# Kernel optimization log

Hardware: AMD Instinct MI355X
Metric: run time of the kernel (lower is better)

The kernel has to match this reference:

```python
import jax, jax.numpy as jnp
import numpy as np

B, N, C = 2, 10000, 128
NH, NP = 4, 20          # n_heads, n_points (n_levels = 1)
DH = C // NH            # head dim = 32
HW = 100                # spatial shape (100, 100), N = HW*HW


def setup_inputs() -> dict:
    key = jax.random.key(0)
    ks = jax.random.split(key, 12)
    s = 0.05  # small param scale so softmax/linears stay well-conditioned
    return {
        "query": jax.random.normal(ks[0], (B, N, C), jnp.float32),
        "query_pos": jax.random.normal(ks[1], (B, N, C), jnp.float32),
        "W_val": jax.random.normal(ks[2], (C, C), jnp.float32) * s,
        "b_val": jax.random.normal(ks[3], (C,), jnp.float32) * s,
        "W_off": jax.random.normal(ks[4], (NH * NP * 2, C), jnp.float32) * s,
        "b_off": jax.random.normal(ks[5], (NH * NP * 2,), jnp.float32) * s,
        "W_attn": jax.random.normal(ks[6], (NH * NP, C), jnp.float32) * s,
        "b_attn": jax.random.normal(ks[7], (NH * NP,), jnp.float32) * s,
        "W_out1": jax.random.normal(ks[8], (C, C), jnp.float32) * s,
        "b_out1": jax.random.normal(ks[9], (C,), jnp.float32) * s,
        "W_out2": jax.random.normal(ks[10], (C, C), jnp.float32) * s,
        "b_out2": jax.random.normal(ks[11], (C,), jnp.float32) * s,
    }


def _msdeform_forward(query, query_pos, W_val, b_val, W_off, b_off,
                      W_attn, b_attn, W_out1, b_out1, W_out2, b_out2):
    residual = query
    q = query + query_pos  # pos added; value branch also uses q (query.clone())

    # reference points: meshgrid of (z, x) normalized to (0,1), shape (N, 2)
    lin = (jnp.arange(HW, dtype=jnp.float32) + 0.5) / HW
    ref_z, ref_x = jnp.meshgrid(lin, lin, indexing="ij")
    ref = jnp.stack([ref_z.reshape(-1), ref_x.reshape(-1)], axis=-1)  # (N,2)

    # projections
    value = (q @ W_val.T + b_val).reshape(B, N, NH, DH).transpose(0, 2, 1, 3)  # (B,NH,N,DH)
    off = (q @ W_off.T + b_off).reshape(B, N, NH, NP, 2)
    attn = jax.nn.softmax((q @ W_attn.T + b_attn).reshape(B, N, NH, NP), axis=-1)

    # sampling locations in normalized coords; offset normalizer = (W, H) = (100, 100)
    loc = ref[None, :, None, None, :] + off / HW  # (B,N,NH,NP,2)

    # grid_sample bilinear, align_corners=False, zeros padding:
    # pixel coord = loc * size - 0.5
    x = (loc[..., 0] * HW - 0.5).transpose(0, 2, 1, 3)  # (B,NH,N,NP)
    y = (loc[..., 1] * HW - 0.5).transpose(0, 2, 1, 3)
    aw = attn.transpose(0, 2, 1, 3)                     # (B,NH,N,NP)

    x0f = jnp.floor(x); y0f = jnp.floor(y)
    wx1 = x - x0f; wy1 = y - y0f
    wx0 = 1.0 - wx1; wy0 = 1.0 - wy1
    ix0 = x0f.astype(jnp.int32); iy0 = y0f.astype(jnp.int32)
    ix1 = ix0 + 1; iy1 = iy0 + 1

    def gather(ix, iy):
        valid = ((ix >= 0) & (ix < HW) & (iy >= 0) & (iy < HW)).astype(value.dtype)
        idx = jnp.clip(iy, 0, HW - 1) * HW + jnp.clip(ix, 0, HW - 1)  # (B,NH,N,NP)
        g = jnp.take_along_axis(value, idx.reshape(B, NH, N * NP, 1), axis=2)
        return g.reshape(B, NH, N, NP, DH) * valid[..., None]

    sampled = ((wx0 * wy0)[..., None] * gather(ix0, iy0)
               + (wx1 * wy0)[..., None] * gather(ix1, iy0)
               + (wx0 * wy1)[..., None] * gather(ix0, iy1)
               + (wx1 * wy1)[..., None] * gather(ix1, iy1))  # (B,NH,N,NP,DH)

    out = (sampled * aw[..., None]).sum(axis=3)             # (B,NH,N,DH)
    out = out.transpose(0, 2, 1, 3).reshape(B, N, C)
    out = out @ W_out1.T + b_out1   # MSDeformAttn.output_proj
    out = out @ W_out2.T + b_out2   # wrapper output_proj
    return out + residual           # dropout is identity in eval


def reference(query, query_pos, W_val, b_val, W_off, b_off,
              W_attn, b_attn, W_out1, b_out1, W_out2, b_out2):
    return _msdeform_forward(query, query_pos, W_val, b_val, W_off, b_off,
                             W_attn, b_attn, W_out1, b_out1, W_out2, b_out2)
```

## Files before the change

kernel.cpp:

```cpp
#include <hip/hip_runtime.h>
#include <hip/hip_bf16.h>
#include <math.h>

#define NTOK 10000
#define BATCH 2
#define CDIM 128
#define NHEAD 4
#define NPNT 20
#define DHEAD 32
#define HWDIM 100
#define MROWS (BATCH * NTOK)
#define OPAD 384
#define PTOK 8
#define PHALO 4
#define PDIM 16
#define NPATCH 13
#define CELLPAD 40

typedef __attribute__((ext_vector_type(8))) short short8v;
typedef __attribute__((ext_vector_type(4))) short short4v;
typedef __attribute__((ext_vector_type(4))) float f32x4;

__device__ __forceinline__ float asf(unsigned u) {
  union { unsigned u; float f; } c; c.u = u; return c.f;
}

__device__ __forceinline__ void acc_cell(const __hip_bfloat16* p, float w,
                                         f32x4& a0, f32x4& a1) {
  int4 u = *(const int4*)p;
  f32x4 g0, g1;
  g0.x = asf(((unsigned)u.x) << 16); g0.y = asf(((unsigned)u.x) & 0xFFFF0000u);
  g0.z = asf(((unsigned)u.y) << 16); g0.w = asf(((unsigned)u.y) & 0xFFFF0000u);
  g1.x = asf(((unsigned)u.z) << 16); g1.y = asf(((unsigned)u.z) & 0xFFFF0000u);
  g1.z = asf(((unsigned)u.w) << 16); g1.w = asf(((unsigned)u.w) & 0xFFFF0000u);
  a0 += g0 * w;
  a1 += g1 * w;
}

__global__ __launch_bounds__(128) void prep_kernel(
    const float* __restrict__ W_val, const float* __restrict__ b_val,
    const float* __restrict__ W_off, const float* __restrict__ b_off,
    const float* __restrict__ W_attn, const float* __restrict__ b_attn,
    const float* __restrict__ W1, const float* __restrict__ b1,
    const float* __restrict__ W2, const float* __restrict__ b2,
    __hip_bfloat16* __restrict__ Wcat, float* __restrict__ bcat,
    __hip_bfloat16* __restrict__ Wc_bf, float* __restrict__ bc) {
  __shared__ float w2row[128];
  __shared__ float red[128];
  const int blk = blockIdx.x, c = threadIdx.x;
  if (blk < OPAD) {
    float v = 0.f, bv = 0.f;
    if (blk < 128) {
      v = W_val[blk * 128 + c]; bv = b_val[blk];
    } else {
      int h = (blk - 128) >> 6, k = (blk - 128) & 63;
      if (k < 40) { v = W_off[(h * 40 + k) * 128 + c]; bv = b_off[h * 40 + k]; }
      else if (k < 60) { v = W_attn[(h * 20 + k - 40) * 128 + c]; bv = b_attn[h * 20 + k - 40]; }
    }
    Wcat[(size_t)blk * 128 + c] = __float2bfloat16(v);
    if (c == 0) bcat[blk] = bv;
  } else {
    const int o = blk - OPAD;
    w2row[c] = W2[o * 128 + c];
    __syncthreads();
    float acc = 0.f;
    for (int k = 0; k < 128; ++k) acc += w2row[k] * W1[k * 128 + c];
    Wc_bf[(size_t)o * 128 + c] = __float2bfloat16(acc);
    red[c] = w2row[c] * b1[c];
    __syncthreads();
    for (int s = 64; s > 0; s >>= 1) {
      if (c < s) red[c] += red[c + s];
      __syncthreads();
    }
    if (c == 0) bc[o] = b2[o] + red[0];
  }
}

__global__ __launch_bounds__(256) void proj1_kernel(
    const float* __restrict__ query, const float* __restrict__ qpos,
    const __hip_bfloat16* __restrict__ Wcat, const float* __restrict__ bcat,
    __hip_bfloat16* __restrict__ value, __hip_bfloat16* __restrict__ offb,
    float* __restrict__ attnb) {
  __shared__ __hip_bfloat16 qa[64][128];
  __shared__ __hip_bfloat16 wb[64][128];
  const int t = threadIdx.x;
  const int r0 = blockIdx.x * 64;

#pragma unroll
  for (int i = 0; i < 4; ++i) {
    int lin = t + 256 * i;
    int r = lin >> 4, g = lin & 15;
    int c = g << 3;
    float4 v0 = make_float4(0.f, 0.f, 0.f, 0.f);
    float4 v1 = make_float4(0.f, 0.f, 0.f, 0.f);
    if (r0 + r < MROWS) {
      const float* p = query + (size_t)(r0 + r) * CDIM + c;
      v0 = *(const float4*)p;
      v1 = *(const float4*)(p + 4);
      const float* p2 = qpos + (size_t)(r0 + r) * CDIM + c;
      float4 u0 = *(const float4*)p2;
      float4 u1 = *(const float4*)(p2 + 4);
      v0.x += u0.x; v0.y += u0.y; v0.z += u0.z; v0.w += u0.w;
      v1.x += u1.x; v1.y += u1.y; v1.z += u1.z; v1.w += u1.w;
    }
    __hip_bfloat16* dst = &qa[r][(g ^ (r & 7)) << 3];
    dst[0] = __float2bfloat16(v0.x); dst[1] = __float2bfloat16(v0.y);
    dst[2] = __float2bfloat16(v0.z); dst[3] = __float2bfloat16(v0.w);
    dst[4] = __float2bfloat16(v1.x); dst[5] = __float2bfloat16(v1.y);
    dst[6] = __float2bfloat16(v1.z); dst[7] = __float2bfloat16(v1.w);
  }
  __syncthreads();

  const int wid = t >> 6;
  const int lane = t & 63;
  const int wr = (wid >> 1) * 32;
  const int wc = (wid & 1) * 32;
  const int lrow = lane & 15;
  const int lk = lane >> 4;

  short8v afr[4][2];
  {
    int ra0 = wr + lrow, ra1 = wr + 16 + lrow;
#pragma unroll
    for (int kk = 0; kk < 4; ++kk) {
      int gb = kk * 4 + lk;
      afr[kk][0] = *(const short8v*)&qa[ra0][(gb ^ (ra0 & 7)) << 3];
      afr[kk][1] = *(const short8v*)&qa[ra1][(gb ^ (ra1 & 7)) << 3];
    }
  }

  for (int ti = 0; ti < 3; ++ti) {
    const int ot = blockIdx.y * 192 + ti * 64;
    __syncthreads();
#pragma unroll
    for (int i = 0; i < 4; ++i) {
      int lin = t + 256 * i;
      int r = lin >> 4, g = lin & 15;
      short8v w = *(const short8v*)(Wcat + (size_t)(ot + r) * 128 + (g << 3));
      *(short8v*)&wb[r][(g ^ (r & 7)) << 3] = w;
    }
    __syncthreads();

    f32x4 acc[2][2];
#pragma unroll
    for (int mi = 0; mi < 2; ++mi)
#pragma unroll
      for (int ni = 0; ni < 2; ++ni) acc[mi][ni] = (f32x4)(0.f);

#pragma unroll
    for (int kk = 0; kk < 4; ++kk) {
      const int gb = kk * 4 + lk;
      int rb0 = wc + lrow, rb1 = wc + 16 + lrow;
      short8v b0 = *(const short8v*)&wb[rb0][(gb ^ (rb0 & 7)) << 3];
      short8v b1 = *(const short8v*)&wb[rb1][(gb ^ (rb1 & 7)) << 3];
      acc[0][0] = __builtin_amdgcn_mfma_f32_16x16x32_bf16(afr[kk][0], b0, acc[0][0], 0, 0, 0);
      acc[0][1] = __builtin_amdgcn_mfma_f32_16x16x32_bf16(afr[kk][0], b1, acc[0][1], 0, 0, 0);
      acc[1][0] = __builtin_amdgcn_mfma_f32_16x16x32_bf16(afr[kk][1], b0, acc[1][0], 0, 0, 0);
      acc[1][1] = __builtin_amdgcn_mfma_f32_16x16x32_bf16(afr[kk][1], b1, acc[1][1], 0, 0, 0);
    }

#pragma unroll
    for (int mi = 0; mi < 2; ++mi) {
#pragma unroll
      for (int ni = 0; ni < 2; ++ni) {
#pragma unroll
        for (int reg = 0; reg < 4; ++reg) {
          int r = r0 + wr + mi * 16 + (lane >> 4) * 4 + reg;
          int o = ot + wc + ni * 16 + (lane & 15);
          if (r >= MROWS) continue;
          float v = acc[mi][ni][reg] + bcat[o];
          int b = r >= NTOK ? 1 : 0;
          int n = r - b * NTOK;
          if (o < 128) {
            int h = o >> 5, rem = o & 31;
            value[(((size_t)b * NHEAD + h) * NTOK + n) * 32 + rem] =
                __float2bfloat16(v);
          } else {
            int h = (o - 128) >> 6, k = (o - 128) & 63;
            size_t base = ((size_t)(b * NHEAD + h) * NTOK + n);
            if (k < 40) {
              offb[base * 40 + k] = __float2bfloat16(v);
            } else if (k < 60) {
              attnb[base * 20 + (k - 40)] = v;
            }
          }
        }
      }
    }
  }
}

__global__ __launch_bounds__(256) void proj2_kernel(
    const __hip_bfloat16* __restrict__ outat,
    const __hip_bfloat16* __restrict__ Wc_bf, const float* __restrict__ bc,
    const float* __restrict__ resid, float* __restrict__ out) {
  __shared__ __hip_bfloat16 qa[64][128];
  __shared__ __hip_bfloat16 wb[64][128];
  const int t = threadIdx.x;
  const int r0 = blockIdx.x * 64;
  const int ot = blockIdx.y * 64;

#pragma unroll
  for (int i = 0; i < 4; ++i) {
    int lin = t + 256 * i;
    int r = lin >> 4, g = lin & 15;
    short8v v = (short8v)(short)0;
    if (r0 + r < MROWS)
      v = *(const short8v*)(outat + (size_t)(r0 + r) * CDIM + (g << 3));
    *(short8v*)&qa[r][(g ^ (r & 7)) << 3] = v;
  }
#pragma unroll
  for (int i = 0; i < 4; ++i) {
    int lin = t + 256 * i;
    int r = lin >> 4, g = lin & 15;
    short8v w = *(const short8v*)(Wc_bf + (size_t)(ot + r) * 128 + (g << 3));
    *(short8v*)&wb[r][(g ^ (r & 7)) << 3] = w;
  }
  __syncthreads();

  const int wid = t >> 6;
  const int lane = t & 63;
  const int wr = (wid >> 1) * 32;
  const int wc = (wid & 1) * 32;
  const int lrow = lane & 15;
  const int lk = lane >> 4;

  f32x4 acc[2][2];
#pragma unroll
  for (int mi = 0; mi < 2; ++mi)
#pragma unroll
    for (int ni = 0; ni < 2; ++ni) acc[mi][ni] = (f32x4)(0.f);

#pragma unroll
  for (int kk = 0; kk < 4; ++kk) {
    const int gb = kk * 4 + lk;
    int ra0 = wr + lrow, ra1 = wr + 16 + lrow;
    int rb0 = wc + lrow, rb1 = wc + 16 + lrow;
    short8v a0 = *(const short8v*)&qa[ra0][(gb ^ (ra0 & 7)) << 3];
    short8v a1 = *(const short8v*)&qa[ra1][(gb ^ (ra1 & 7)) << 3];
    short8v b0 = *(const short8v*)&wb[rb0][(gb ^ (rb0 & 7)) << 3];
    short8v b1 = *(const short8v*)&wb[rb1][(gb ^ (rb1 & 7)) << 3];
    acc[0][0] = __builtin_amdgcn_mfma_f32_16x16x32_bf16(a0, b0, acc[0][0], 0, 0, 0);
    acc[0][1] = __builtin_amdgcn_mfma_f32_16x16x32_bf16(a0, b1, acc[0][1], 0, 0, 0);
    acc[1][0] = __builtin_amdgcn_mfma_f32_16x16x32_bf16(a1, b0, acc[1][0], 0, 0, 0);
    acc[1][1] = __builtin_amdgcn_mfma_f32_16x16x32_bf16(a1, b1, acc[1][1], 0, 0, 0);
  }

#pragma unroll
  for (int mi = 0; mi < 2; ++mi) {
#pragma unroll
    for (int ni = 0; ni < 2; ++ni) {
#pragma unroll
      for (int reg = 0; reg < 4; ++reg) {
        int r = r0 + wr + mi * 16 + (lane >> 4) * 4 + reg;
        int o = ot + wc + ni * 16 + (lane & 15);
        if (r >= MROWS) continue;
        out[(size_t)r * CDIM + o] =
            acc[mi][ni][reg] + bc[o] + resid[(size_t)r * CDIM + o];
      }
    }
  }
}

__global__ __launch_bounds__(256) void sample_kernel(
    const __hip_bfloat16* __restrict__ value,
    const __hip_bfloat16* __restrict__ off, const float* __restrict__ attn,
    __hip_bfloat16* __restrict__ outat) {
  const int s = blockIdx.x & 7;
  const int pidx = blockIdx.x >> 3;
  const int PI = pidx % NPATCH, PJ = pidx / NPATCH;
  const int I0 = PI * PTOK, J0 = PJ * PTOK;
  const int b = s >> 2, h = s & 3;

  __shared__ __hip_bfloat16 patch[PDIM * PDIM][CELLPAD];
  const __hip_bfloat16* vglob = value + (size_t)s * NTOK * DHEAD;

  const int dl = threadIdx.x & 3;
  const int tok = threadIdx.x >> 2;
  const int li = tok & 7, lj = tok >> 3;
  const int i = I0 + li, j = J0 + lj;
  const bool tv = (i < HWDIM) && (j < HWDIM);
  const int n = tv ? (i * HWDIM + j) : 0;
  union { int4 v4[5]; unsigned u[20]; } of;
  union { float4 v4[5]; float f[20]; } at;
  {
    const int4* o4 = (const int4*)(off + ((size_t)s * NTOK + n) * 40);
    const float4* a4 = (const float4*)(attn + ((size_t)s * NTOK + n) * 20);
#pragma unroll
    for (int q = 0; q < 5; ++q) of.v4[q] = o4[q];
#pragma unroll
    for (int q = 0; q < 5; ++q) at.v4[q] = a4[q];
  }

#pragma unroll
  for (int it = 0; it < 4; ++it) {
    int lin = threadIdx.x + 256 * it;
    int cell = lin >> 2, part = lin & 3;
    int py = cell >> 4, px = cell & 15;
    int gy = J0 - PHALO + py;
    int gx = I0 - PHALO + px;
    short8v v = (short8v)(short)0;
    if (gy >= 0 && gy < HWDIM && gx >= 0 && gx < HWDIM)
      v = *(const short8v*)(vglob + ((size_t)(gy * HWDIM + gx)) * DHEAD +
                            part * 8);
    *(short8v*)&patch[cell][part * 8] = v;
  }
  __syncthreads();

  if (!tv) return;

  float ssum = 0.f;
#pragma unroll
  for (int p = 0; p < NPNT; ++p) {
    at.f[p] = __expf(at.f[p]);
    ssum += at.f[p];
  }
  const float inv = 1.f / ssum;

  const float fi = (float)i, fj = (float)j;
  f32x4 c0a = (f32x4)(0.f), c0b = (f32x4)(0.f);
  f32x4 c1a = (f32x4)(0.f), c1b = (f32x4)(0.f);
  f32x4 c2a = (f32x4)(0.f), c2b = (f32x4)(0.f);
  f32x4 c3a = (f32x4)(0.f), c3b = (f32x4)(0.f);
#pragma unroll
  for (int p = 0; p < NPNT; ++p) {
    const unsigned up = of.u[p];
    float x = fi + asf(up << 16);
    float y = fj + asf(up & 0xFFFF0000u);
    float aw = at.f[p];
    float x0f = floorf(x), y0f = floorf(y);
    int ix0 = (int)x0f, iy0 = (int)y0f;
    float wx1 = x - x0f, wy1 = y - y0f;
    float wx0 = 1.f - wx1, wy0 = 1.f - wy1;
    float wya = aw * wy0, wyb = aw * wy1;
    float w00 = wya * wx0, w01 = wya * wx1;
    float w10 = wyb * wx0, w11 = wyb * wx1;
    int ly = iy0 - (J0 - PHALO);
    int lx = ix0 - (I0 - PHALO);
    if ((unsigned)ly <= PDIM - 2 && (unsigned)lx <= PDIM - 2) {
      const __hip_bfloat16* pb = &patch[ly * PDIM + lx][dl * 8];
      acc_cell(pb, w00, c0a, c0b);
      acc_cell(pb + CELLPAD, w01, c1a, c1b);
      acc_cell(pb + PDIM * CELLPAD, w10, c2a, c2b);
      acc_cell(pb + PDIM * CELLPAD + CELLPAD, w11, c3a, c3b);
    } else {
      float wgt[4] = {w00, w01, w10, w11};
#pragma unroll
      for (int cy = 0; cy < 2; ++cy) {
        int iy = iy0 + cy;
        if (iy < 0 || iy >= HWDIM) continue;
#pragma unroll
        for (int cx = 0; cx < 2; ++cx) {
          int ix = ix0 + cx;
          if (ix < 0 || ix >= HWDIM) continue;
          acc_cell(vglob + ((size_t)(iy * HWDIM + ix)) * DHEAD + dl * 8,
                   wgt[cy * 2 + cx], c0a, c0b);
        }
      }
    }
  }
  f32x4 a0 = (c0a + c1a) + (c2a + c3a);
  f32x4 a1 = (c0b + c1b) + (c2b + c3b);

  union { short8v v8; __hip_bfloat16 hh[8]; } o;
#pragma unroll
  for (int k = 0; k < 4; ++k) {
    o.hh[k] = __float2bfloat16(a0[k] * inv);
    o.hh[4 + k] = __float2bfloat16(a1[k] * inv);
  }
  *(short8v*)(outat + ((size_t)b * NTOK + n) * CDIM + h * DHEAD + dl * 8) =
      o.v8;
}

extern "C" void kernel_launch(void* const* d_in, const int* in_sizes, int n_in,
                              void* d_out, int out_size, void* d_ws,
                              size_t ws_size, hipStream_t stream) {
  const float* query = (const float*)d_in[0];
  const float* query_pos = (const float*)d_in[1];
  const float* W_val = (const float*)d_in[2];
  const float* b_val = (const float*)d_in[3];
  const float* W_off = (const float*)d_in[4];
  const float* b_off = (const float*)d_in[5];
  const float* W_attn = (const float*)d_in[6];
  const float* b_attn = (const float*)d_in[7];
  const float* W_out1 = (const float*)d_in[8];
  const float* b_out1 = (const float*)d_in[9];
  const float* W_out2 = (const float*)d_in[10];
  const float* b_out2 = (const float*)d_in[11];
  float* out = (float*)d_out;

  char* ws = (char*)d_ws;
  __hip_bfloat16* value = (__hip_bfloat16*)ws;
  ws += (size_t)MROWS * CDIM * 2;
  __hip_bfloat16* offb = (__hip_bfloat16*)ws;
  ws += (size_t)MROWS * 160 * 2;
  float* attnb = (float*)ws;
  ws += (size_t)MROWS * 80 * 4;
  __hip_bfloat16* outat = (__hip_bfloat16*)ws;
  ws += (size_t)MROWS * CDIM * 2;
  float* bcat = (float*)ws; ws += OPAD * 4;
  float* bc = (float*)ws; ws += 128 * 4;
  __hip_bfloat16* Wcat = (__hip_bfloat16*)ws; ws += (size_t)OPAD * 128 * 2;
  __hip_bfloat16* Wc_bf = (__hip_bfloat16*)ws;

  prep_kernel<<<OPAD + 128, 128, 0, stream>>>(
      W_val, b_val, W_off, b_off, W_attn, b_attn, W_out1, b_out1, W_out2,
      b_out2, Wcat, bcat, Wc_bf, bc);

  proj1_kernel<<<dim3(313, 2), 256, 0, stream>>>(query, query_pos, Wcat, bcat,
                                                 value, offb, attnb);

  sample_kernel<<<8 * NPATCH * NPATCH, 256, 0, stream>>>(value, offb, attnb,
                                                         outat);

  proj2_kernel<<<dim3(313, 2), 256, 0, stream>>>(outat, Wc_bf, bc, query, out);
}
```

Baseline: 61.61 us.

## Split sampling points across lanes with smaller 4x4 token tiles and shuffle reduction

The sampling kernel now assigns 16 threads per token: 4 point-groups of 5 points times 4 channel groups. Partial sums and the softmax denominator are combined with xor shuffles. Tiles shrink from 8x8 to 4x4 tokens with a 12x12 shared patch, giving 625 tiles per head-batch instead of 169. This raises parallelism, cuts per-thread serial work and removes idle threads at tile edges. The cost is a larger share of halo loads per token, more blocks, and shuffle overhead.

Result: faster. 58.95 us, median of 2 (-4.3%).

```diff
diff --git a/kernel.cpp b/kernel.cpp
--- a/kernel.cpp
+++ b/kernel.cpp
@@ -11,10 +11,10 @@
 #define HWDIM 100
 #define MROWS (BATCH * NTOK)
 #define OPAD 384
-#define PTOK 8
 #define PHALO 4
-#define PDIM 16
-#define NPATCH 13
+#define TTILE 4
+#define SPD 12
+#define NPT 25
 #define CELLPAD 40
 
 typedef __attribute__((ext_vector_type(8))) short short8v;
@@ -268,66 +268,65 @@
     __hip_bfloat16* __restrict__ outat) {
   const int s = blockIdx.x & 7;
   const int pidx = blockIdx.x >> 3;
-  const int PI = pidx % NPATCH, PJ = pidx / NPATCH;
-  const int I0 = PI * PTOK, J0 = PJ * PTOK;
+  const int PI = pidx % NPT, PJ = pidx / NPT;
+  const int I0 = PI * TTILE, J0 = PJ * TTILE;
   const int b = s >> 2, h = s & 3;
 
-  __shared__ __hip_bfloat16 patch[PDIM * PDIM][CELLPAD];
+  __shared__ __hip_bfloat16 patch[SPD * SPD][CELLPAD];
   const __hip_bfloat16* vglob = value + (size_t)s * NTOK * DHEAD;
 
-  const int dl = threadIdx.x & 3;
-  const int tok = threadIdx.x >> 2;
-  const int li = tok & 7, lj = tok >> 3;
+  const int t = threadIdx.x;
+  const int lane16 = t & 15;
+  const int dg = lane16 & 3;
+  const int pg = lane16 >> 2;
+  const int tok = t >> 4;
+  const int li = tok & 3, lj = tok >> 2;
   const int i = I0 + li, j = J0 + lj;
-  const bool tv = (i < HWDIM) && (j < HWDIM);
-  const int n = tv ? (i * HWDIM + j) : 0;
-  union { int4 v4[5]; unsigned u[20]; } of;
-  union { float4 v4[5]; float f[20]; } at;
+  const int n = i * HWDIM + j;
+
+  unsigned ofu[5];
+  float atf[5];
   {
-    const int4* o4 = (const int4*)(off + ((size_t)s * NTOK + n) * 40);
-    const float4* a4 = (const float4*)(attn + ((size_t)s * NTOK + n) * 20);
-#pragma unroll
-    for (int q = 0; q < 5; ++q) of.v4[q] = o4[q];
-#pragma unroll
-    for (int q = 0; q < 5; ++q) at.v4[q] = a4[q];
-  }
-
-#pragma unroll
-  for (int it = 0; it < 4; ++it) {
-    int lin = threadIdx.x + 256 * it;
-    int cell = lin >> 2, part = lin & 3;
-    int py = cell >> 4, px = cell & 15;
-    int gy = J0 - PHALO + py;
-    int gx = I0 - PHALO + px;
-    short8v v = (short8v)(short)0;
-    if (gy >= 0 && gy < HWDIM && gx >= 0 && gx < HWDIM)
-      v = *(const short8v*)(vglob + ((size_t)(gy * HWDIM + gx)) * DHEAD +
-                            part * 8);
-    *(short8v*)&patch[cell][part * 8] = v;
+    const unsigned* ob =
+        (const unsigned*)(off + ((size_t)s * NTOK + n) * 40) + pg * 5;
+    const float* ab = attn + ((size_t)s * NTOK + n) * 20 + pg * 5;
+#pragma unroll
+    for (int k = 0; k < 5; ++k) { ofu[k] = ob[k]; atf[k] = ab[k]; }
+  }
+
+#pragma unroll
+  for (int it = 0; it < 3; ++it) {
+    int lin = t + 256 * it;
+    if (lin < SPD * SPD * 4) {
+      int cell = lin >> 2, part = lin & 3;
+      int py = cell / SPD, px = cell - py * SPD;
+      int gy = J0 - PHALO + py;
+      int gx = I0 - PHALO + px;
+      short8v v = (short8v)(short)0;
+      if (gy >= 0 && gy < HWDIM && gx >= 0 && gx < HWDIM)
+        v = *(const short8v*)(vglob + ((size_t)(gy * HWDIM + gx)) * DHEAD +
+                              part * 8);
+      *(short8v*)&patch[cell][part * 8] = v;
+    }
   }
   __syncthreads();
 
-  if (!tv) return;
-
   float ssum = 0.f;
 #pragma unroll
-  for (int p = 0; p < NPNT; ++p) {
-    at.f[p] = __expf(at.f[p]);
-    ssum += at.f[p];
-  }
-  const float inv = 1.f / ssum;
+  for (int k = 0; k < 5; ++k) {
+    atf[k] = __expf(atf[k]);
+    ssum += atf[k];
+  }
 
   const float fi = (float)i, fj = (float)j;
-  f32x4 c0a = (f32x4)(0.f), c0b = (f32x4)(0.f);
-  f32x4 c1a = (f32x4)(0.f), c1b = (f32x4)(0.f);
-  f32x4 c2a = (f32x4)(0.f), c2b = (f32x4)(0.f);
-  f32x4 c3a = (f32x4)(0.f), c3b = (f32x4)(0.f);
-#pragma unroll
-  for (int p = 0; p < NPNT; ++p) {
-    const unsigned up = of.u[p];
+  f32x4 a0 = (f32x4)(0.f), a1 = (f32x4)(0.f);
+  f32x4 e0 = (f32x4)(0.f), e1 = (f32x4)(0.f);
+#pragma unroll
+  for (int k = 0; k < 5; ++k) {
+    const unsigned up = ofu[k];
     float x = fi + asf(up << 16);
     float y = fj + asf(up & 0xFFFF0000u);
-    float aw = at.f[p];
+    float aw = atf[k];
     float x0f = floorf(x), y0f = floorf(y);
     int ix0 = (int)x0f, iy0 = (int)y0f;
     float wx1 = x - x0f, wy1 = y - y0f;
@@ -337,12 +336,12 @@
     float w10 = wyb * wx0, w11 = wyb * wx1;
     int ly = iy0 - (J0 - PHALO);
     int lx = ix0 - (I0 - PHALO);
-    if ((unsigned)ly <= PDIM - 2 && (unsigned)lx <= PDIM - 2) {
-      const __hip_bfloat16* pb = &patch[ly * PDIM + lx][dl * 8];
-      acc_cell(pb, w00, c0a, c0b);
-      acc_cell(pb + CELLPAD, w01, c1a, c1b);
-      acc_cell(pb + PDIM * CELLPAD, w10, c2a, c2b);
-      acc_cell(pb + PDIM * CELLPAD + CELLPAD, w11, c3a, c3b);
+    if ((unsigned)ly <= SPD - 2 && (unsigned)lx <= SPD - 2) {
+      const __hip_bfloat16* pb = &patch[ly * SPD + lx][dg * 8];
+      acc_cell(pb, w00, a0, a1);
+      acc_cell(pb + CELLPAD, w01, e0, e1);
+      acc_cell(pb + SPD * CELLPAD, w10, a0, a1);
+      acc_cell(pb + SPD * CELLPAD + CELLPAD, w11, e0, e1);
     } else {
       float wgt[4] = {w00, w01, w10, w11};
 #pragma unroll
@@ -353,23 +352,36 @@
         for (int cx = 0; cx < 2; ++cx) {
           int ix = ix0 + cx;
           if (ix < 0 || ix >= HWDIM) continue;
-          acc_cell(vglob + ((size_t)(iy * HWDIM + ix)) * DHEAD + dl * 8,
-                   wgt[cy * 2 + cx], c0a, c0b);
+          acc_cell(vglob + ((size_t)(iy * HWDIM + ix)) * DHEAD + dg * 8,
+                   wgt[cy * 2 + cx], a0, a1);
         }
       }
     }
   }
-  f32x4 a0 = (c0a + c1a) + (c2a + c3a);
-  f32x4 a1 = (c0b + c1b) + (c2b + c3b);
-
-  union { short8v v8; __hip_bfloat16 hh[8]; } o;
-#pragma unroll
-  for (int k = 0; k < 4; ++k) {
-    o.hh[k] = __float2bfloat16(a0[k] * inv);
-    o.hh[4 + k] = __float2bfloat16(a1[k] * inv);
-  }
-  *(short8v*)(outat + ((size_t)b * NTOK + n) * CDIM + h * DHEAD + dl * 8) =
-      o.v8;
+  f32x4 r0 = a0 + e0;
+  f32x4 r1 = a1 + e1;
+
+#pragma unroll
+  for (int m = 4; m <= 8; m <<= 1) {
+#pragma unroll
+    for (int el = 0; el < 4; ++el) {
+      r0[el] += __shfl_xor(r0[el], m);
+      r1[el] += __shfl_xor(r1[el], m);
+    }
+    ssum += __shfl_xor(ssum, m);
+  }
+
+  if (pg == 0) {
+    const float inv = 1.f / ssum;
+    union { short8v v8; __hip_bfloat16 hh[8]; } o;
+#pragma unroll
+    for (int k = 0; k < 4; ++k) {
+      o.hh[k] = __float2bfloat16(r0[k] * inv);
+      o.hh[4 + k] = __float2bfloat16(r1[k] * inv);
+    }
+    *(short8v*)(outat + ((size_t)b * NTOK + n) * CDIM + h * DHEAD + dg * 8) =
+        o.v8;
+  }
 }
 
 extern "C" void kernel_launch(void* const* d_in, const int* in_sizes, int n_in,
@@ -410,8 +422,7 @@
   proj1_kernel<<<dim3(313, 2), 256, 0, stream>>>(query, query_pos, Wcat, bcat,
                                                  value, offb, attnb);
 
-  sample_kernel<<<8 * NPATCH * NPATCH, 256, 0, stream>>>(value, offb, attnb,
-                                                         outat);
+  sample_kernel<<<8 * NPT * NPT, 256, 0, stream>>>(value, offb, attnb, outat);
 
   proj2_kernel<<<dim3(313, 2), 256, 0, stream>>>(outat, Wc_bf, bc, query, out);
 }
```
